# Optimization experiments

Measured on AMD Instinct MI355X. Metric: run time of the kernel, lower is better.

Reference implementation:

```python
import jax, jax.numpy as jnp
from jax import lax
import numpy as np

G, K = 8, 9  # deformable groups, 3x3 kernel taps


def conv1x1_bn_relu(x, W, scale, bias):
    # Conv2d 1x1 (no bias) + folded eval-mode BatchNorm (per-channel scale/bias) + ReLU
    y = jnp.einsum('bchw,oc->bohw', x, W)
    return jax.nn.relu(y * scale[None, :, None, None] + bias[None, :, None, None])


def dcn_v2(feat, offset_feat, W_om, b_om, W_dcn, b_dcn):
    # Modulated deformable conv v2, 3x3, stride 1, pad 1, dilation 1,
    # deformable_groups=G, extra_offset_mask: offsets/mask predicted from offset_feat.
    B, C, H, W_ = feat.shape
    Cg = C // G
    om = lax.conv_general_dilated(offset_feat, W_om, (1, 1), ((1, 1), (1, 1)))
    om = om + b_om[None, :, None, None]              # [B, 3*G*K, H, W]
    o1, o2, m = jnp.split(om, 3, axis=1)
    off_y = o1.reshape(B, G, K, H, W_)
    off_x = o2.reshape(B, G, K, H, W_)
    mask = jax.nn.sigmoid(m).reshape(B, G, K, H, W_)
    dk = jnp.arange(3) - 1
    dkh = jnp.repeat(dk, 3)   # tap row offset,  k = kh*3 + kw
    dkw = jnp.tile(dk, 3)     # tap col offset
    hh = jnp.arange(H, dtype=feat.dtype)
    ww = jnp.arange(W_, dtype=feat.dtype)
    py = hh[None, None, None, :, None] + dkh[None, None, :, None, None].astype(feat.dtype) + off_y
    px = ww[None, None, None, None, :] + dkw[None, None, :, None, None].astype(feat.dtype) + off_x
    y0 = jnp.floor(py); x0 = jnp.floor(px)
    ty = py - y0; tx = px - x0
    xg = feat.reshape(B, G, Cg, H * W_)

    def gather(idx):  # idx [B,G,K,H,W] int32 -> [B,G,Cg,K,H,W]
        f = lambda xf, i: xf[:, i]
        return jax.vmap(jax.vmap(f))(xg, idx)

    val = jnp.zeros((B, G, Cg, K, H, W_), dtype=feat.dtype)
    y0i = y0.astype(jnp.int32); x0i = x0.astype(jnp.int32)
    for dy, wy in ((0, 1.0 - ty), (1, ty)):
        iy = y0i + dy
        vy = (iy >= 0) & (iy < H)
        iyc = jnp.clip(iy, 0, H - 1)
        for dx, wx in ((0, 1.0 - tx), (1, tx)):
            ix = x0i + dx
            v = vy & (ix >= 0) & (ix < W_)
            idx = iyc * W_ + jnp.clip(ix, 0, W_ - 1)
            w = (wy * wx) * v.astype(feat.dtype)      # zero-padding outside
            val = val + w[:, :, None] * gather(idx)
    val = val * mask[:, :, None]                      # modulation
    Wd = W_dcn.reshape(W_dcn.shape[0], G, Cg, K)      # [Cout, G, Cg, K]
    out = jnp.einsum('bgckhw,ogck->bohw', val, Wd) + b_dcn[None, :, None, None]
    return out


def setup_inputs() -> dict:
    key = jax.random.key(0)
    ks = jax.random.split(key, 16)
    B, C, H, W_ = 8, 128, 64, 64
    Cd = C // 2  # dcn out channels = 64
    d = {}
    d['feat_l'] = jax.random.normal(ks[0], (B, C, H, W_), jnp.float32)
    d['feat_s'] = jax.random.normal(ks[1], (B, C, H // 2, W_ // 2), jnp.float32)
    d['W_fsm'] = jax.random.normal(ks[2], (C, C), jnp.float32) / np.sqrt(C)
    d['s_fsm'] = 1.0 + 0.1 * jax.random.normal(ks[3], (C,), jnp.float32)
    d['b_fsm'] = 0.1 * jax.random.normal(ks[4], (C,), jnp.float32)
    d['W_off'] = jax.random.normal(ks[5], (C, 2 * C), jnp.float32) / np.sqrt(2 * C)
    d['s_off'] = 1.0 + 0.1 * jax.random.normal(ks[6], (C,), jnp.float32)
    d['b_off'] = 0.1 * jax.random.normal(ks[7], (C,), jnp.float32)
    d['W_om'] = 0.05 * jax.random.normal(ks[8], (3 * G * K, C, 3, 3), jnp.float32)
    d['b_om'] = jnp.zeros((3 * G * K,), jnp.float32)
    d['W_dcn'] = jax.random.normal(ks[9], (Cd, C, 3, 3), jnp.float32) / np.sqrt(C * 9)
    d['b_dcn'] = 0.1 * jax.random.normal(ks[10], (Cd,), jnp.float32)
    d['W_cat'] = jax.random.normal(ks[11], (C, Cd), jnp.float32) / np.sqrt(Cd)
    d['s_cat'] = 1.0 + 0.1 * jax.random.normal(ks[12], (C,), jnp.float32)
    d['b_cat'] = 0.1 * jax.random.normal(ks[13], (C,), jnp.float32)
    return d


def reference(feat_l, feat_s, W_fsm, s_fsm, b_fsm, W_off, s_off, b_off,
              W_om, b_om, W_dcn, b_dcn, W_cat, s_cat, b_cat):
    # nearest upsample x2 (F.interpolate nearest to feat_l spatial size)
    feat_up = jnp.repeat(jnp.repeat(feat_s, 2, axis=2), 2, axis=3)
    feat_arm = conv1x1_bn_relu(feat_l, W_fsm, s_fsm, b_fsm)
    offset = conv1x1_bn_relu(jnp.concatenate([feat_arm, feat_up * 2.0], axis=1),
                             W_off, s_off, b_off)
    feat_align = jax.nn.relu(dcn_v2(feat_up, offset, W_om, b_om, W_dcn, b_dcn))
    feat = conv1x1_bn_relu(feat_align, W_cat, s_cat, b_cat) + feat_arm
    return (feat, feat_arm)
```

## Files before the change

### kernel.cpp

```cpp
#include <hip/hip_runtime.h>


typedef __attribute__((ext_vector_type(8))) short short8;
typedef __attribute__((ext_vector_type(4))) float f32x4;
typedef _Float16 __attribute__((ext_vector_type(2))) h2;

static __device__ __forceinline__ unsigned short f2bf(float x) {
    union { float f; unsigned int u; } v; v.f = x;
    return (unsigned short)((v.u + 0x7FFF + ((v.u >> 16) & 1)) >> 16);
}
static __device__ __forceinline__ unsigned short f2h(float x) {
    union { _Float16 h; unsigned short u; } v; v.h = (_Float16)x;
    return v.u;
}

__global__ __launch_bounds__(256) void k_prepfs(const float* __restrict__ fs,
        uint4* __restrict__ fsT4, uint4* __restrict__ fsH4) {
    __shared__ unsigned short st[64 * 136];
    unsigned int* st32 = (unsigned int*)st;
    const int t = threadIdx.x;
    const int b = blockIdx.x >> 4;
    const int p0 = (blockIdx.x & 15) << 6;
    for (int i = t; i < 64 * 64; i += 256) {
        int c2 = i >> 6, px = i & 63;
        float v0 = fs[(((b << 7) + 2 * c2) << 10) + p0 + px];
        float v1 = fs[(((b << 7) + 2 * c2 + 1) << 10) + p0 + px];
        st32[px * 68 + c2] = (unsigned int)f2bf(v0) | ((unsigned int)f2bf(v1) << 16);
    }
    __syncthreads();
    for (int i = t; i < 64 * 16; i += 256) {
        int px = i >> 4, q = i & 15;
        fsT4[(((b << 10) + p0 + px) << 4) + q] = ((const uint4*)(st + px * 136))[q];
    }
    __syncthreads();
    for (int i = t; i < 64 * 64; i += 256) {
        int c2 = i >> 6, px = i & 63;
        float v0 = fs[(((b << 7) + 2 * c2) << 10) + p0 + px];
        float v1 = fs[(((b << 7) + 2 * c2 + 1) << 10) + p0 + px];
        st32[px * 68 + c2] = (unsigned int)f2h(v0) | ((unsigned int)f2h(v1) << 16);
    }
    __syncthreads();
    for (int i = t; i < 64 * 16; i += 256) {
        int px = i >> 4, q = i & 15;
        fsH4[(((b << 10) + p0 + px) << 4) + q] = ((const uint4*)(st + px * 136))[q];
    }
}

__global__ __launch_bounds__(256) void k_packall(
        const float* __restrict__ W_fsm, const float* __restrict__ W_off,
        const float* __restrict__ W_cat, const float* __restrict__ W_dcn,
        const float* __restrict__ W_om,
        unsigned short* __restrict__ wbfsm, unsigned short* __restrict__ wboff,
        unsigned short* __restrict__ wbcat, unsigned short* __restrict__ wbdcn,
        unsigned short* __restrict__ wb2) {
    int idx = blockIdx.x * 256 + threadIdx.x;
    int lane = idx & 63;
    int ml = lane & 15, kl = (lane >> 4) * 8;
    unsigned short tmp[8];
    if (idx < 2048) {
        int r = idx >> 6;
        int o = (r % 8) * 16 + ml, k0 = (r / 8) * 32 + kl;
#pragma unroll
        for (int j = 0; j < 8; j++) tmp[j] = f2bf(W_fsm[o * 128 + k0 + j]);
        ((uint4*)wbfsm)[idx] = *(const uint4*)tmp;
    } else if (idx < 6144) {
        int i2 = idx - 2048;
        int r = i2 >> 6;
        int o = (r % 8) * 16 + ml, k0 = (r / 8) * 32 + kl;
#pragma unroll
        for (int j = 0; j < 8; j++) {
            int k = k0 + j;
            float f = W_off[o * 256 + k];
            if (k >= 128) f *= 2.0f;
            tmp[j] = f2bf(f);
        }
        ((uint4*)wboff)[i2] = *(const uint4*)tmp;
    } else if (idx < 7168) {
        int i2 = idx - 6144;
        int r = i2 >> 6;
        int o = (r % 8) * 16 + ml, k0 = (r / 8) * 32 + kl;
#pragma unroll
        for (int j = 0; j < 8; j++) tmp[j] = f2bf(W_cat[o * 64 + k0 + j]);
        ((uint4*)wbcat)[i2] = *(const uint4*)tmp;
    } else if (idx < 16384) {
        int i2 = idx - 7168;
        int r = i2 >> 6;
        int o = (r & 3) * 16 + ml, k0 = (r >> 2) * 32 + kl;
#pragma unroll
        for (int j = 0; j < 8; j++) {
            int k = k0 + j;
            int g = k / 144;
            int rem = k - g * 144;
            tmp[j] = f2h(W_dcn[(o * 128 + g * 16 + (rem & 15)) * 9 + (rem >> 4)]);
        }
        ((uint4*)wbdcn)[i2] = *(const uint4*)tmp;
    } else if (idx < 53248) {
        int i2 = idx - 16384;
        int r = i2 >> 6;
        int nt = r & 15, kk = r >> 4;
        int tap = kk >> 2, cc = kk & 3;
        int o = nt * 16 + ml;
        int c0 = cc * 32 + kl;
#pragma unroll
        for (int j = 0; j < 8; j++) {
            float v = (o < 216) ? W_om[(o * 128 + (c0 + j)) * 9 + tap] : 0.0f;
            tmp[j] = f2bf(v);
        }
        ((uint4*)wb2)[i2] = *(const uint4*)tmp;
    }
}

__global__ __launch_bounds__(256) void k12(const float* __restrict__ feat_l,
        const uint4* __restrict__ fsT4,
        const unsigned short* __restrict__ wbf, const unsigned short* __restrict__ wbo,
        const float* __restrict__ s_fsm, const float* __restrict__ b_fsm,
        const float* __restrict__ s_off, const float* __restrict__ b_off,
        float* __restrict__ feat_arm, unsigned short* __restrict__ offT) {
    __shared__ unsigned short A1[64 * 136];
    __shared__ unsigned short A2[64 * 264];
    float* E32 = (float*)A1;
    const int t = threadIdx.x;
    const int b = blockIdx.x >> 6;
    const int h = blockIdx.x & 63;
    const int hw0 = h << 6;
    unsigned int* A1w = (unsigned int*)A1;
    for (int i = t; i < 64 * 64; i += 256) {
        int c2 = i >> 6, px = i & 63;
        float v0 = feat_l[(((b << 7) + 2 * c2) << 12) + hw0 + px];
        float v1 = feat_l[(((b << 7) + 2 * c2 + 1) << 12) + hw0 + px];
        A1w[px * 68 + c2] = (unsigned int)f2bf(v0) | ((unsigned int)f2bf(v1) << 16);
    }
    {
        const int h2 = h >> 1;
        for (int i = t; i < 32 * 16; i += 256) {
            int px2 = i >> 4, q = i & 15;
            uint4 v = fsT4[(((b << 10) + (h2 << 5) + px2) << 4) + q];
            ((uint4*)(A2 + (2 * px2) * 264 + 128))[q] = v;
            ((uint4*)(A2 + (2 * px2 + 1) * 264 + 128))[q] = v;
        }
    }
    __syncthreads();
    const int lane = t & 63;
    const int wid = __builtin_amdgcn_readfirstlane(t >> 6);
    const int m = lane & 15, ko = lane >> 4;
    f32x4 acc[8];
#pragma unroll
    for (int nt = 0; nt < 8; nt++) acc[nt] = (f32x4){0.f, 0.f, 0.f, 0.f};
#pragma unroll
    for (int kk = 0; kk < 4; kk++) {
        short8 av = *(const short8*)(A1 + (wid * 16 + m) * 136 + kk * 32 + ko * 8);
        const uint4* wb = (const uint4*)wbf + (kk * 8) * 64 + lane;
#pragma unroll
        for (int nt = 0; nt < 8; nt++) {
            uint4 bu = wb[nt * 64];
            acc[nt] = __builtin_amdgcn_mfma_f32_16x16x32_bf16(av, *(short8*)&bu, acc[nt], 0, 0, 0);
        }
    }
#pragma unroll
    for (int nt = 0; nt < 8; nt++) {
        int o = nt * 16 + m;
        float sc = s_fsm[o], bi = b_fsm[o];
#pragma unroll
        for (int r = 0; r < 4; r++) {
            float v = fmaf(acc[nt][r], sc, bi);
            v = v > 0.f ? v : 0.f;
            acc[nt][r] = v;
            A2[(wid * 16 + ko * 4 + r) * 264 + o] = f2bf(v);
        }
    }
#pragma unroll 1
    for (int half = 0; half < 2; half++) {
        __syncthreads();
#pragma unroll
        for (int nt2 = 0; nt2 < 4; nt2++) {
            int nt = half * 4 + nt2;
#pragma unroll
            for (int r = 0; r < 4; r++)
                E32[(wid * 16 + ko * 4 + r) * 67 + nt2 * 16 + m] = acc[nt][r];
        }
        __syncthreads();
        for (int i = t; i < 4096; i += 256) {
            int ol = i >> 6, pp = i & 63;
            feat_arm[(((b << 7) + half * 64 + ol) << 12) + hw0 + pp] = E32[pp * 67 + ol];
        }
    }
    __syncthreads();
    f32x4 acc2[8];
#pragma unroll
    for (int nt = 0; nt < 8; nt++) acc2[nt] = (f32x4){0.f, 0.f, 0.f, 0.f};
#pragma unroll
    for (int kk = 0; kk < 8; kk++) {
        short8 av = *(const short8*)(A2 + (wid * 16 + m) * 264 + kk * 32 + ko * 8);
        const uint4* wb = (const uint4*)wbo + (kk * 8) * 64 + lane;
#pragma unroll
        for (int nt = 0; nt < 8; nt++) {
            uint4 bu = wb[nt * 64];
            acc2[nt] = __builtin_amdgcn_mfma_f32_16x16x32_bf16(av, *(short8*)&bu, acc2[nt], 0, 0, 0);
        }
    }
    __syncthreads();
#pragma unroll
    for (int nt = 0; nt < 8; nt++) {
        int o = nt * 16 + m;
        float sc = s_off[o], bi = b_off[o];
#pragma unroll
        for (int r = 0; r < 4; r++) {
            float v = fmaf(acc2[nt][r], sc, bi);
            v = v > 0.f ? v : 0.f;
            A2[(wid * 16 + ko * 4 + r) * 264 + o] = f2bf(v);
        }
    }
    __syncthreads();
    for (int i = t; i < 64 * 16; i += 256) {
        int px = i >> 4, q = i & 15;
        ((uint4*)offT)[(((b << 12) + hw0 + px) << 4) + q] = ((const uint4*)(A2 + px * 264))[q];
    }
}

__global__ __launch_bounds__(256, 2) void k_omdcn(
        const unsigned short* __restrict__ offT, const uint4* __restrict__ fsH4,
        const unsigned short* __restrict__ Wb2, const float* __restrict__ bom,
        const unsigned short* __restrict__ wbd, const float* __restrict__ bd,
        const unsigned short* __restrict__ wbc,
        const float* __restrict__ s_cat, const float* __restrict__ b_cat,
        const float* __restrict__ feat_arm, float* __restrict__ feat) {
    __shared__ float LDSf[16384];
    unsigned short* st = (unsigned short*)LDSf;
    float* omT = LDSf;
    unsigned short* A3 = (unsigned short*)(LDSf + 13888);
    float* T = LDSf;
    const uint4* offT4 = (const uint4*)offT;
    const uint4* W4 = (const uint4*)Wb2;
    const int t = threadIdx.x;
    const int b = blockIdx.x >> 6;
    const int h = blockIdx.x & 63;
    for (int i = t; i < 3 * 66 * 16; i += 256) {
        int q = i & 15;
        int rp = i >> 4;
        int r = rp / 66, p = rp - r * 66;
        int gy = h + r - 1, gx = p - 1;
        uint4 v = make_uint4(0, 0, 0, 0);
        if (gy >= 0 && gy < 64 && gx >= 0 && gx < 64)
            v = offT4[((((b << 6) + gy) << 6) + gx) * 16 + q];
        ((uint4*)(st + rp * 136))[q] = v;
    }
    __syncthreads();
    const int lane = t & 63;
    const int wid = __builtin_amdgcn_readfirstlane(t >> 6);
    const int m = lane & 15, ko = lane >> 4;
    f32x4 acc[16];
#pragma unroll
    for (int i = 0; i < 16; i++) acc[i] = (f32x4){0.f, 0.f, 0.f, 0.f};
#pragma unroll 4
    for (int kk = 0; kk < 36; kk++) {
        const int tap = kk >> 2, cc = kk & 3;
        const int dy = tap / 3, dx = tap - dy * 3;
        uint4 b4[4];
#pragma unroll
        for (int nt2 = 0; nt2 < 4; nt2++)
            b4[nt2] = W4[(((kk << 4) + (wid << 2) + nt2) << 6) + lane];
        short8 a8[4];
#pragma unroll
        for (int mt = 0; mt < 4; mt++) {
            int p = mt * 16 + m + dx;
            a8[mt] = *(const short8*)(st + (dy * 66 + p) * 136 + (cc << 5) + (ko << 3));
        }
#pragma unroll
        for (int nt2 = 0; nt2 < 4; nt2++)
#pragma unroll
            for (int mt = 0; mt < 4; mt++)
                acc[nt2 * 4 + mt] = __builtin_amdgcn_mfma_f32_16x16x32_bf16(
                    a8[mt], *(short8*)&b4[nt2], acc[nt2 * 4 + mt], 0, 0, 0);
    }
    __syncthreads();
#pragma unroll
    for (int nt2 = 0; nt2 < 4; nt2++) {
        int o = ((wid * 4 + nt2) << 4) + m;
        if (o < 216) {
            float bv = bom[o];
#pragma unroll
            for (int mt = 0; mt < 4; mt++) {
                f32x4 v = acc[nt2 * 4 + mt];
#pragma unroll
                for (int r = 0; r < 4; r++)
                    omT[(mt * 16 + (ko << 2) + r) * 217 + o] = v[r] + bv;
            }
        }
    }
    __syncthreads();
    const int px = (wid << 4) + m;
    const float fh = (float)h, fw = (float)px;
    const int pb_ = b << 10;
    const float* omrow = omT + px * 217;
    f32x4 accd[4];
#pragma unroll
    for (int nt = 0; nt < 4; nt++) accd[nt] = (f32x4){0.f, 0.f, 0.f, 0.f};
#pragma unroll
    for (int kk = 0; kk < 36; kk++) {
        int k0 = (kk << 5) + (ko << 3);
        int g = k0 / 144;
        int rem = k0 - g * 144;
        int tap = rem >> 4;
        int c0 = rem & 15;
        int ch = g * 9 + tap;
        float oy = omrow[ch];
        float ox = omrow[72 + ch];
        float mmv = omrow[144 + ch];
        mmv = 1.0f / (1.0f + __expf(-mmv));
        float py = fh + (float)(tap / 3 - 1) + oy;
        float pxx = fw + (float)(tap % 3 - 1) + ox;
        float y0f = floorf(py), x0f = floorf(pxx);
        float tyf = py - y0f, txf = pxx - x0f;
        int y0i = (int)y0f, x0i = (int)x0f;
        int y1i = y0i + 1, x1i = x0i + 1;
        bool vy0 = (y0i >= 0) && (y0i < 64);
        bool vy1 = (y1i >= 0) && (y1i < 64);
        bool vx0 = (x0i >= 0) && (x0i < 64);
        bool vx1 = (x1i >= 0) && (x1i < 64);
        float w00 = (vy0 && vx0) ? (1.0f - tyf) * (1.0f - txf) * mmv : 0.0f;
        float w01 = (vy0 && vx1) ? (1.0f - tyf) * txf * mmv : 0.0f;
        float w10 = (vy1 && vx0) ? tyf * (1.0f - txf) * mmv : 0.0f;
        float w11 = (vy1 && vx1) ? tyf * txf * mmv : 0.0f;
        int yc0 = y0i < 0 ? 0 : (y0i > 63 ? 63 : y0i);
        int yc1 = y1i < 0 ? 0 : (y1i > 63 ? 63 : y1i);
        int xc0 = x0i < 0 ? 0 : (x0i > 63 ? 63 : x0i);
        int xc1 = x1i < 0 ? 0 : (x1i > 63 ? 63 : x1i);
        int row0 = (yc0 >> 1) << 5, row1 = (yc1 >> 1) << 5;
        int ci = g * 2 + (c0 >> 3);
        union { uint4 u; h2 h[4]; } C00, C01, C10, C11;
        C00.u = fsH4[((pb_ + row0 + (xc0 >> 1)) << 4) + ci];
        C01.u = fsH4[((pb_ + row0 + (xc1 >> 1)) << 4) + ci];
        C10.u = fsH4[((pb_ + row1 + (xc0 >> 1)) << 4) + ci];
        C11.u = fsH4[((pb_ + row1 + (xc1 >> 1)) << 4) + ci];
        _Float16 h00 = (_Float16)w00, h01 = (_Float16)w01;
        _Float16 h10 = (_Float16)w10, h11 = (_Float16)w11;
        h2 W00 = (h2){h00, h00}, W01 = (h2){h01, h01};
        h2 W10 = (h2){h10, h10}, W11 = (h2){h11, h11};
        union { short8 s; h2 h[4]; } av;
#pragma unroll
        for (int c = 0; c < 4; c++)
            av.h[c] = C00.h[c] * W00 + C01.h[c] * W01 + C10.h[c] * W10 + C11.h[c] * W11;
        const uint4* wb = (const uint4*)wbd + (kk << 2) * 64 + lane;
#pragma unroll
        for (int nt = 0; nt < 4; nt++) {
            uint4 bu = wb[nt * 64];
            accd[nt] = __builtin_amdgcn_mfma_f32_16x16x32_f16(av.s, *(short8*)&bu, accd[nt], 0, 0, 0);
        }
    }
#pragma unroll
    for (int nt = 0; nt < 4; nt++) {
        int o = (nt << 4) + m;
        float bv = bd[o];
#pragma unroll
        for (int r = 0; r < 4; r++) {
            float v = accd[nt][r] + bv;
            v = v > 0.f ? v : 0.f;
            A3[((wid << 4) + (ko << 2) + r) * 72 + o] = f2bf(v);
        }
    }
    f32x4 acc2[8];
#pragma unroll
    for (int nt = 0; nt < 8; nt++) acc2[nt] = (f32x4){0.f, 0.f, 0.f, 0.f};
#pragma unroll
    for (int kk2 = 0; kk2 < 2; kk2++) {
        short8 av = *(const short8*)(A3 + ((wid << 4) + m) * 72 + kk2 * 32 + (ko << 3));
#pragma unroll
        for (int nt2 = 0; nt2 < 8; nt2++) {
            uint4 bu = ((const uint4*)wbc)[(kk2 * 8 + nt2) * 64 + lane];
            acc2[nt2] = __builtin_amdgcn_mfma_f32_16x16x32_bf16(av, *(short8*)&bu, acc2[nt2], 0, 0, 0);
        }
    }
#pragma unroll 1
    for (int half = 0; half < 2; half++) {
        __syncthreads();
#pragma unroll
        for (int nt2l = 0; nt2l < 4; nt2l++) {
            int nt2 = half * 4 + nt2l;
            int o = (nt2 << 4) + m;
            float sc = s_cat[o], bi = b_cat[o];
#pragma unroll
            for (int r = 0; r < 4; r++) {
                float v = fmaf(acc2[nt2][r], sc, bi);
                v = v > 0.f ? v : 0.f;
                T[((wid << 4) + (ko << 2) + r) * 67 + (nt2l << 4) + m] = v;
            }
        }
        __syncthreads();
        for (int i = t; i < 4096; i += 256) {
            int ol = i >> 6, pp = i & 63;
            int gidx = (((b << 7) + half * 64 + ol) << 12) + (h << 6) + pp;
            feat[gidx] = T[pp * 67 + ol] + feat_arm[gidx];
        }
    }
}

extern "C" void kernel_launch(void* const* d_in, const int* in_sizes, int n_in,
                              void* d_out, int out_size, void* d_ws, size_t ws_size,
                              hipStream_t stream) {
    const float* feat_l = (const float*)d_in[0];
    const float* feat_s = (const float*)d_in[1];
    const float* W_fsm  = (const float*)d_in[2];
    const float* s_fsm  = (const float*)d_in[3];
    const float* b_fsm  = (const float*)d_in[4];
    const float* W_off  = (const float*)d_in[5];
    const float* s_off  = (const float*)d_in[6];
    const float* b_off  = (const float*)d_in[7];
    const float* W_om   = (const float*)d_in[8];
    const float* b_om   = (const float*)d_in[9];
    const float* W_dcn  = (const float*)d_in[10];
    const float* b_dcn  = (const float*)d_in[11];
    const float* W_cat  = (const float*)d_in[12];
    const float* s_cat  = (const float*)d_in[13];
    const float* b_cat  = (const float*)d_in[14];

    float* feat     = (float*)d_out;
    float* feat_arm = feat + 4194304;

    float* ws = (float*)d_ws;
    unsigned short* offT = (unsigned short*)ws;
    uint4* fsT4  = (uint4*)(ws + 9175040);
    unsigned short* wb2   = (unsigned short*)(ws + 9699328);
    unsigned short* wbfsm = (unsigned short*)(ws + 9846784);
    unsigned short* wboff = (unsigned short*)(ws + 9854976);
    unsigned short* wbcat = (unsigned short*)(ws + 9871360);
    unsigned short* wbdcn = (unsigned short*)(ws + 9875456);
    uint4* fsH4  = (uint4*)(ws + 9912320);

    k_prepfs<<<128, 256, 0, stream>>>(feat_s, fsT4, fsH4);
    k_packall<<<208, 256, 0, stream>>>(W_fsm, W_off, W_cat, W_dcn, W_om,
                                       wbfsm, wboff, wbcat, wbdcn, wb2);

    k12<<<512, 256, 0, stream>>>(feat_l, fsT4, wbfsm, wboff,
                                 s_fsm, b_fsm, s_off, b_off, feat_arm, offT);
    k_omdcn<<<512, 256, 0, stream>>>(offT, fsH4, wb2, b_om, wbdcn, b_dcn,
                                     wbcat, s_cat, b_cat, feat_arm, feat);
}
```

Measured before the change: 188.0 us.

## Double block size to 512 threads with split-K and split-N wave partitioning

Both main kernels move from 256 to 512 threads per block. In k12 the extra waves split the output channels between two wave groups. In k_omdcn they split the K dimension of the offset conv and the deformable conv into halves, reduce partial sums through LDS, and split the N dimension of the final 1x1 conv. The aim is more waves per block to hide the latency of the gather and the MFMAs, and a shorter serial K loop per wave. In exchange it adds extra LDS reduction passes and barriers, and register limits under the launch bounds of (512,4) may cause spills.

Measured after the change: 176.2 us. -6.3%, faster.

```diff
diff --git a/kernel.cpp b/kernel.cpp
--- a/kernel.cpp
+++ b/kernel.cpp
@@ -110,7 +110,7 @@
     }
 }
 
-__global__ __launch_bounds__(256) void k12(const float* __restrict__ feat_l,
+__global__ __launch_bounds__(512, 4) void k12(const float* __restrict__ feat_l,
         const uint4* __restrict__ fsT4,
         const unsigned short* __restrict__ wbf, const unsigned short* __restrict__ wbo,
         const float* __restrict__ s_fsm, const float* __restrict__ b_fsm,
@@ -124,7 +124,7 @@
     const int h = blockIdx.x & 63;
     const int hw0 = h << 6;
     unsigned int* A1w = (unsigned int*)A1;
-    for (int i = t; i < 64 * 64; i += 256) {
+    for (int i = t; i < 64 * 64; i += 512) {
         int c2 = i >> 6, px = i & 63;
         float v0 = feat_l[(((b << 7) + 2 * c2) << 12) + hw0 + px];
         float v1 = feat_l[(((b << 7) + 2 * c2 + 1) << 12) + hw0 + px];
@@ -132,92 +132,92 @@
     }
     {
         const int h2 = h >> 1;
-        for (int i = t; i < 32 * 16; i += 256) {
-            int px2 = i >> 4, q = i & 15;
-            uint4 v = fsT4[(((b << 10) + (h2 << 5) + px2) << 4) + q];
-            ((uint4*)(A2 + (2 * px2) * 264 + 128))[q] = v;
-            ((uint4*)(A2 + (2 * px2 + 1) * 264 + 128))[q] = v;
-        }
+        int px2 = t >> 4, q = t & 15;
+        uint4 v = fsT4[(((b << 10) + (h2 << 5) + px2) << 4) + q];
+        ((uint4*)(A2 + (2 * px2) * 264 + 128))[q] = v;
+        ((uint4*)(A2 + (2 * px2 + 1) * 264 + 128))[q] = v;
     }
     __syncthreads();
     const int lane = t & 63;
-    const int wid = __builtin_amdgcn_readfirstlane(t >> 6);
+    const int w = __builtin_amdgcn_readfirstlane(t >> 6);
+    const int pq = w & 3;
+    const int nh = w >> 2;
     const int m = lane & 15, ko = lane >> 4;
-    f32x4 acc[8];
-#pragma unroll
-    for (int nt = 0; nt < 8; nt++) acc[nt] = (f32x4){0.f, 0.f, 0.f, 0.f};
+    f32x4 acc[4];
+#pragma unroll
+    for (int nt2 = 0; nt2 < 4; nt2++) acc[nt2] = (f32x4){0.f, 0.f, 0.f, 0.f};
 #pragma unroll
     for (int kk = 0; kk < 4; kk++) {
-        short8 av = *(const short8*)(A1 + (wid * 16 + m) * 136 + kk * 32 + ko * 8);
-        const uint4* wb = (const uint4*)wbf + (kk * 8) * 64 + lane;
-#pragma unroll
-        for (int nt = 0; nt < 8; nt++) {
-            uint4 bu = wb[nt * 64];
-            acc[nt] = __builtin_amdgcn_mfma_f32_16x16x32_bf16(av, *(short8*)&bu, acc[nt], 0, 0, 0);
-        }
-    }
-#pragma unroll
-    for (int nt = 0; nt < 8; nt++) {
-        int o = nt * 16 + m;
+        short8 av = *(const short8*)(A1 + (pq * 16 + m) * 136 + kk * 32 + ko * 8);
+        const uint4* wb = (const uint4*)wbf + (kk * 8 + nh * 4) * 64 + lane;
+#pragma unroll
+        for (int nt2 = 0; nt2 < 4; nt2++) {
+            uint4 bu = wb[nt2 * 64];
+            acc[nt2] = __builtin_amdgcn_mfma_f32_16x16x32_bf16(av, *(short8*)&bu, acc[nt2], 0, 0, 0);
+        }
+    }
+#pragma unroll
+    for (int nt2 = 0; nt2 < 4; nt2++) {
+        int o = ((nh << 2) + nt2) * 16 + m;
         float sc = s_fsm[o], bi = b_fsm[o];
 #pragma unroll
         for (int r = 0; r < 4; r++) {
-            float v = fmaf(acc[nt][r], sc, bi);
+            float v = fmaf(acc[nt2][r], sc, bi);
             v = v > 0.f ? v : 0.f;
-            acc[nt][r] = v;
-            A2[(wid * 16 + ko * 4 + r) * 264 + o] = f2bf(v);
+            acc[nt2][r] = v;
+            A2[(pq * 16 + ko * 4 + r) * 264 + o] = f2bf(v);
         }
     }
 #pragma unroll 1
     for (int half = 0; half < 2; half++) {
         __syncthreads();
-#pragma unroll
-        for (int nt2 = 0; nt2 < 4; nt2++) {
-            int nt = half * 4 + nt2;
-#pragma unroll
-            for (int r = 0; r < 4; r++)
-                E32[(wid * 16 + ko * 4 + r) * 67 + nt2 * 16 + m] = acc[nt][r];
+        if (nh == half) {
+#pragma unroll
+            for (int nt2 = 0; nt2 < 4; nt2++)
+#pragma unroll
+                for (int r = 0; r < 4; r++)
+                    E32[(pq * 16 + ko * 4 + r) * 67 + nt2 * 16 + m] = acc[nt2][r];
         }
         __syncthreads();
-        for (int i = t; i < 4096; i += 256) {
+        for (int i = t; i < 4096; i += 512) {
             int ol = i >> 6, pp = i & 63;
             feat_arm[(((b << 7) + half * 64 + ol) << 12) + hw0 + pp] = E32[pp * 67 + ol];
         }
     }
     __syncthreads();
-    f32x4 acc2[8];
-#pragma unroll
-    for (int nt = 0; nt < 8; nt++) acc2[nt] = (f32x4){0.f, 0.f, 0.f, 0.f};
+    f32x4 acc2[4];
+#pragma unroll
+    for (int nt2 = 0; nt2 < 4; nt2++) acc2[nt2] = (f32x4){0.f, 0.f, 0.f, 0.f};
 #pragma unroll
     for (int kk = 0; kk < 8; kk++) {
-        short8 av = *(const short8*)(A2 + (wid * 16 + m) * 264 + kk * 32 + ko * 8);
-        const uint4* wb = (const uint4*)wbo + (kk * 8) * 64 + lane;
-#pragma unroll
-        for (int nt = 0; nt < 8; nt++) {
-            uint4 bu = wb[nt * 64];
-            acc2[nt] = __builtin_amdgcn_mfma_f32_16x16x32_bf16(av, *(short8*)&bu, acc2[nt], 0, 0, 0);
-        }
-    }
-    __syncthreads();
-#pragma unroll
-    for (int nt = 0; nt < 8; nt++) {
-        int o = nt * 16 + m;
+        short8 av = *(const short8*)(A2 + (pq * 16 + m) * 264 + kk * 32 + ko * 8);
+        const uint4* wb = (const uint4*)wbo + (kk * 8 + nh * 4) * 64 + lane;
+#pragma unroll
+        for (int nt2 = 0; nt2 < 4; nt2++) {
+            uint4 bu = wb[nt2 * 64];
+            acc2[nt2] = __builtin_amdgcn_mfma_f32_16x16x32_bf16(av, *(short8*)&bu, acc2[nt2], 0, 0, 0);
+        }
+    }
+    __syncthreads();
+#pragma unroll
+    for (int nt2 = 0; nt2 < 4; nt2++) {
+        int o = ((nh << 2) + nt2) * 16 + m;
         float sc = s_off[o], bi = b_off[o];
 #pragma unroll
         for (int r = 0; r < 4; r++) {
-            float v = fmaf(acc2[nt][r], sc, bi);
+            float v = fmaf(acc2[nt2][r], sc, bi);
             v = v > 0.f ? v : 0.f;
-            A2[(wid * 16 + ko * 4 + r) * 264 + o] = f2bf(v);
-        }
-    }
-    __syncthreads();
-    for (int i = t; i < 64 * 16; i += 256) {
+            A2[(pq * 16 + ko * 4 + r) * 264 + o] = f2bf(v);
+        }
+    }
+    __syncthreads();
+    for (int i = t; i < 64 * 16; i += 512) {
         int px = i >> 4, q = i & 15;
         ((uint4*)offT)[(((b << 12) + hw0 + px) << 4) + q] = ((const uint4*)(A2 + px * 264))[q];
     }
 }
 
-__global__ __launch_bounds__(256, 2) void k_omdcn(
+__global__ __launch_bounds__(512, 4) void k_omdcn(
         const unsigned short* __restrict__ offT, const uint4* __restrict__ fsH4,
         const unsigned short* __restrict__ Wb2, const float* __restrict__ bom,
         const unsigned short* __restrict__ wbd, const float* __restrict__ bd,
@@ -227,6 +227,7 @@
     __shared__ float LDSf[16384];
     unsigned short* st = (unsigned short*)LDSf;
     float* omT = LDSf;
+    float* Rbuf = LDSf;
     unsigned short* A3 = (unsigned short*)(LDSf + 13888);
     float* T = LDSf;
     const uint4* offT4 = (const uint4*)offT;
@@ -234,7 +235,7 @@
     const int t = threadIdx.x;
     const int b = blockIdx.x >> 6;
     const int h = blockIdx.x & 63;
-    for (int i = t; i < 3 * 66 * 16; i += 256) {
+    for (int i = t; i < 3 * 66 * 16; i += 512) {
         int q = i & 15;
         int rp = i >> 4;
         int r = rp / 66, p = rp - r * 66;
@@ -246,147 +247,189 @@
     }
     __syncthreads();
     const int lane = t & 63;
-    const int wid = __builtin_amdgcn_readfirstlane(t >> 6);
+    const int w = __builtin_amdgcn_readfirstlane(t >> 6);
+    const int nq = w & 3;
+    const int kh = w >> 2;
     const int m = lane & 15, ko = lane >> 4;
     f32x4 acc[16];
 #pragma unroll
     for (int i = 0; i < 16; i++) acc[i] = (f32x4){0.f, 0.f, 0.f, 0.f};
+    {
+        const int kk0 = kh * 18;
 #pragma unroll 4
-    for (int kk = 0; kk < 36; kk++) {
-        const int tap = kk >> 2, cc = kk & 3;
-        const int dy = tap / 3, dx = tap - dy * 3;
-        uint4 b4[4];
-#pragma unroll
-        for (int nt2 = 0; nt2 < 4; nt2++)
-            b4[nt2] = W4[(((kk << 4) + (wid << 2) + nt2) << 6) + lane];
-        short8 a8[4];
-#pragma unroll
-        for (int mt = 0; mt < 4; mt++) {
-            int p = mt * 16 + m + dx;
-            a8[mt] = *(const short8*)(st + (dy * 66 + p) * 136 + (cc << 5) + (ko << 3));
-        }
-#pragma unroll
-        for (int nt2 = 0; nt2 < 4; nt2++)
-#pragma unroll
-            for (int mt = 0; mt < 4; mt++)
-                acc[nt2 * 4 + mt] = __builtin_amdgcn_mfma_f32_16x16x32_bf16(
-                    a8[mt], *(short8*)&b4[nt2], acc[nt2 * 4 + mt], 0, 0, 0);
-    }
-    __syncthreads();
-#pragma unroll
-    for (int nt2 = 0; nt2 < 4; nt2++) {
-        int o = ((wid * 4 + nt2) << 4) + m;
-        if (o < 216) {
-            float bv = bom[o];
+        for (int kki = 0; kki < 18; kki++) {
+            const int kk = kk0 + kki;
+            const int tap = kk >> 2, cc = kk & 3;
+            const int dy = tap / 3, dx = tap - dy * 3;
+            uint4 b4[4];
+#pragma unroll
+            for (int nt2 = 0; nt2 < 4; nt2++)
+                b4[nt2] = W4[(((kk << 4) + (nq << 2) + nt2) << 6) + lane];
+            short8 a8[4];
 #pragma unroll
             for (int mt = 0; mt < 4; mt++) {
-                f32x4 v = acc[nt2 * 4 + mt];
-#pragma unroll
-                for (int r = 0; r < 4; r++)
-                    omT[(mt * 16 + (ko << 2) + r) * 217 + o] = v[r] + bv;
-            }
-        }
-    }
-    __syncthreads();
-    const int px = (wid << 4) + m;
+                int p = mt * 16 + m + dx;
+                a8[mt] = *(const short8*)(st + (dy * 66 + p) * 136 + (cc << 5) + (ko << 3));
+            }
+#pragma unroll
+            for (int nt2 = 0; nt2 < 4; nt2++)
+#pragma unroll
+                for (int mt = 0; mt < 4; mt++)
+                    acc[nt2 * 4 + mt] = __builtin_amdgcn_mfma_f32_16x16x32_bf16(
+                        a8[mt], *(short8*)&b4[nt2], acc[nt2 * 4 + mt], 0, 0, 0);
+        }
+    }
+    __syncthreads();
+    if (kh == 0) {
+#pragma unroll
+        for (int nt2 = 0; nt2 < 4; nt2++) {
+            int o = ((nq << 2) + nt2) * 16 + m;
+            if (o < 216) {
+                float bv = bom[o];
+#pragma unroll
+                for (int mt = 0; mt < 4; mt++) {
+                    f32x4 v = acc[nt2 * 4 + mt];
+#pragma unroll
+                    for (int r = 0; r < 4; r++)
+                        omT[(mt * 16 + (ko << 2) + r) * 217 + o] = v[r] + bv;
+                }
+            }
+        }
+    }
+    __syncthreads();
+    if (kh == 1) {
+#pragma unroll
+        for (int nt2 = 0; nt2 < 4; nt2++) {
+            int o = ((nq << 2) + nt2) * 16 + m;
+            if (o < 216) {
+#pragma unroll
+                for (int mt = 0; mt < 4; mt++) {
+                    f32x4 v = acc[nt2 * 4 + mt];
+#pragma unroll
+                    for (int r = 0; r < 4; r++)
+                        omT[(mt * 16 + (ko << 2) + r) * 217 + o] += v[r];
+                }
+            }
+        }
+    }
+    __syncthreads();
+    const int px = (nq << 4) + m;
     const float fh = (float)h, fw = (float)px;
     const int pb_ = b << 10;
     const float* omrow = omT + px * 217;
     f32x4 accd[4];
 #pragma unroll
     for (int nt = 0; nt < 4; nt++) accd[nt] = (f32x4){0.f, 0.f, 0.f, 0.f};
-#pragma unroll
-    for (int kk = 0; kk < 36; kk++) {
-        int k0 = (kk << 5) + (ko << 3);
-        int g = k0 / 144;
-        int rem = k0 - g * 144;
-        int tap = rem >> 4;
-        int c0 = rem & 15;
-        int ch = g * 9 + tap;
-        float oy = omrow[ch];
-        float ox = omrow[72 + ch];
-        float mmv = omrow[144 + ch];
-        mmv = 1.0f / (1.0f + __expf(-mmv));
-        float py = fh + (float)(tap / 3 - 1) + oy;
-        float pxx = fw + (float)(tap % 3 - 1) + ox;
-        float y0f = floorf(py), x0f = floorf(pxx);
-        float tyf = py - y0f, txf = pxx - x0f;
-        int y0i = (int)y0f, x0i = (int)x0f;
-        int y1i = y0i + 1, x1i = x0i + 1;
-        bool vy0 = (y0i >= 0) && (y0i < 64);
-        bool vy1 = (y1i >= 0) && (y1i < 64);
-        bool vx0 = (x0i >= 0) && (x0i < 64);
-        bool vx1 = (x1i >= 0) && (x1i < 64);
-        float w00 = (vy0 && vx0) ? (1.0f - tyf) * (1.0f - txf) * mmv : 0.0f;
-        float w01 = (vy0 && vx1) ? (1.0f - tyf) * txf * mmv : 0.0f;
-        float w10 = (vy1 && vx0) ? tyf * (1.0f - txf) * mmv : 0.0f;
-        float w11 = (vy1 && vx1) ? tyf * txf * mmv : 0.0f;
-        int yc0 = y0i < 0 ? 0 : (y0i > 63 ? 63 : y0i);
-        int yc1 = y1i < 0 ? 0 : (y1i > 63 ? 63 : y1i);
-        int xc0 = x0i < 0 ? 0 : (x0i > 63 ? 63 : x0i);
-        int xc1 = x1i < 0 ? 0 : (x1i > 63 ? 63 : x1i);
-        int row0 = (yc0 >> 1) << 5, row1 = (yc1 >> 1) << 5;
-        int ci = g * 2 + (c0 >> 3);
-        union { uint4 u; h2 h[4]; } C00, C01, C10, C11;
-        C00.u = fsH4[((pb_ + row0 + (xc0 >> 1)) << 4) + ci];
-        C01.u = fsH4[((pb_ + row0 + (xc1 >> 1)) << 4) + ci];
-        C10.u = fsH4[((pb_ + row1 + (xc0 >> 1)) << 4) + ci];
-        C11.u = fsH4[((pb_ + row1 + (xc1 >> 1)) << 4) + ci];
-        _Float16 h00 = (_Float16)w00, h01 = (_Float16)w01;
-        _Float16 h10 = (_Float16)w10, h11 = (_Float16)w11;
-        h2 W00 = (h2){h00, h00}, W01 = (h2){h01, h01};
-        h2 W10 = (h2){h10, h10}, W11 = (h2){h11, h11};
-        union { short8 s; h2 h[4]; } av;
-#pragma unroll
-        for (int c = 0; c < 4; c++)
-            av.h[c] = C00.h[c] * W00 + C01.h[c] * W01 + C10.h[c] * W10 + C11.h[c] * W11;
-        const uint4* wb = (const uint4*)wbd + (kk << 2) * 64 + lane;
+    {
+        const int dk0 = kh * 18;
+#pragma unroll
+        for (int kki = 0; kki < 18; kki++) {
+            const int kk = dk0 + kki;
+            int k0 = (kk << 5) + (ko << 3);
+            int g = k0 / 144;
+            int rem = k0 - g * 144;
+            int tap = rem >> 4;
+            int c0 = rem & 15;
+            int ch = g * 9 + tap;
+            float oy = omrow[ch];
+            float ox = omrow[72 + ch];
+            float mmv = omrow[144 + ch];
+            mmv = 1.0f / (1.0f + __expf(-mmv));
+            float py = fh + (float)(tap / 3 - 1) + oy;
+            float pxx = fw + (float)(tap % 3 - 1) + ox;
+            float y0f = floorf(py), x0f = floorf(pxx);
+            float tyf = py - y0f, txf = pxx - x0f;
+            int y0i = (int)y0f, x0i = (int)x0f;
+            int y1i = y0i + 1, x1i = x0i + 1;
+            bool vy0 = (y0i >= 0) && (y0i < 64);
+            bool vy1 = (y1i >= 0) && (y1i < 64);
+            bool vx0 = (x0i >= 0) && (x0i < 64);
+            bool vx1 = (x1i >= 0) && (x1i < 64);
+            float w00 = (vy0 && vx0) ? (1.0f - tyf) * (1.0f - txf) * mmv : 0.0f;
+            float w01 = (vy0 && vx1) ? (1.0f - tyf) * txf * mmv : 0.0f;
+            float w10 = (vy1 && vx0) ? tyf * (1.0f - txf) * mmv : 0.0f;
+            float w11 = (vy1 && vx1) ? tyf * txf * mmv : 0.0f;
+            int yc0 = y0i < 0 ? 0 : (y0i > 63 ? 63 : y0i);
+            int yc1 = y1i < 0 ? 0 : (y1i > 63 ? 63 : y1i);
+            int xc0 = x0i < 0 ? 0 : (x0i > 63 ? 63 : x0i);
+            int xc1 = x1i < 0 ? 0 : (x1i > 63 ? 63 : x1i);
+            int row0 = (yc0 >> 1) << 5, row1 = (yc1 >> 1) << 5;
+            int ci = g * 2 + (c0 >> 3);
+            union { uint4 u; h2 h[4]; } C00, C01, C10, C11;
+            C00.u = fsH4[((pb_ + row0 + (xc0 >> 1)) << 4) + ci];
+            C01.u = fsH4[((pb_ + row0 + (xc1 >> 1)) << 4) + ci];
+            C10.u = fsH4[((pb_ + row1 + (xc0 >> 1)) << 4) + ci];
+            C11.u = fsH4[((pb_ + row1 + (xc1 >> 1)) << 4) + ci];
+            _Float16 h00 = (_Float16)w00, h01 = (_Float16)w01;
+            _Float16 h10 = (_Float16)w10, h11 = (_Float16)w11;
+            h2 W00 = (h2){h00, h00}, W01 = (h2){h01, h01};
+            h2 W10 = (h2){h10, h10}, W11 = (h2){h11, h11};
+            union { short8 s; h2 h[4]; } av;
+#pragma unroll
+            for (int c = 0; c < 4; c++)
+                av.h[c] = C00.h[c] * W00 + C01.h[c] * W01 + C10.h[c] * W10 + C11.h[c] * W11;
+            const uint4* wb = (const uint4*)wbd + (kk << 2) * 64 + lane;
+#pragma unroll
+            for (int nt = 0; nt < 4; nt++) {
+                uint4 bu = wb[nt * 64];
+                accd[nt] = __builtin_amdgcn_mfma_f32_16x16x32_f16(av.s, *(short8*)&bu, accd[nt], 0, 0, 0);
+            }
+        }
+    }
+    __syncthreads();
+    if (kh == 1) {
+#pragma unroll
+        for (int nt = 0; nt < 4; nt++)
+            *(f32x4*)(Rbuf + ((nq << 6) + lane) * 20 + (nt << 2)) = accd[nt];
+    }
+    __syncthreads();
+    if (kh == 0) {
+#pragma unroll
+        for (int nt = 0; nt < 4; nt++)
+            accd[nt] += *(const f32x4*)(Rbuf + ((nq << 6) + lane) * 20 + (nt << 2));
 #pragma unroll
         for (int nt = 0; nt < 4; nt++) {
-            uint4 bu = wb[nt * 64];
-            accd[nt] = __builtin_amdgcn_mfma_f32_16x16x32_f16(av.s, *(short8*)&bu, accd[nt], 0, 0, 0);
-        }
-    }
-#pragma unroll
-    for (int nt = 0; nt < 4; nt++) {
-        int o = (nt << 4) + m;
-        float bv = bd[o];
-#pragma unroll
-        for (int r = 0; r < 4; r++) {
-            float v = accd[nt][r] + bv;
-            v = v > 0.f ? v : 0.f;
-            A3[((wid << 4) + (ko << 2) + r) * 72 + o] = f2bf(v);
-        }
-    }
-    f32x4 acc2[8];
-#pragma unroll
-    for (int nt = 0; nt < 8; nt++) acc2[nt] = (f32x4){0.f, 0.f, 0.f, 0.f};
+            int o = (nt << 4) + m;
+            float bv = bd[o];
+#pragma unroll
+            for (int r = 0; r < 4; r++) {
+                float v = accd[nt][r] + bv;
+                v = v > 0.f ? v : 0.f;
+                A3[((nq << 4) + (ko << 2) + r) * 72 + o] = f2bf(v);
+            }
+        }
+    }
+    __syncthreads();
+    f32x4 acc2[4];
+#pragma unroll
+    for (int nt2 = 0; nt2 < 4; nt2++) acc2[nt2] = (f32x4){0.f, 0.f, 0.f, 0.f};
 #pragma unroll
     for (int kk2 = 0; kk2 < 2; kk2++) {
-        short8 av = *(const short8*)(A3 + ((wid << 4) + m) * 72 + kk2 * 32 + (ko << 3));
-#pragma unroll
-        for (int nt2 = 0; nt2 < 8; nt2++) {
-            uint4 bu = ((const uint4*)wbc)[(kk2 * 8 + nt2) * 64 + lane];
+        short8 av = *(const short8*)(A3 + ((nq << 4) + m) * 72 + kk2 * 32 + (ko << 3));
+#pragma unroll
+        for (int nt2 = 0; nt2 < 4; nt2++) {
+            uint4 bu = ((const uint4*)wbc)[(kk2 * 8 + (kh << 2) + nt2) * 64 + lane];
             acc2[nt2] = __builtin_amdgcn_mfma_f32_16x16x32_bf16(av, *(short8*)&bu, acc2[nt2], 0, 0, 0);
         }
     }
 #pragma unroll 1
     for (int half = 0; half < 2; half++) {
         __syncthreads();
-#pragma unroll
-        for (int nt2l = 0; nt2l < 4; nt2l++) {
-            int nt2 = half * 4 + nt2l;
-            int o = (nt2 << 4) + m;
-            float sc = s_cat[o], bi = b_cat[o];
-#pragma unroll
-            for (int r = 0; r < 4; r++) {
-                float v = fmaf(acc2[nt2][r], sc, bi);
-                v = v > 0.f ? v : 0.f;
-                T[((wid << 4) + (ko << 2) + r) * 67 + (nt2l << 4) + m] = v;
+        if (kh == half) {
+#pragma unroll
+            for (int nt2 = 0; nt2 < 4; nt2++) {
+                int o = (((kh << 2) + nt2) << 4) + m;
+                float sc = s_cat[o], bi = b_cat[o];
+#pragma unroll
+                for (int r = 0; r < 4; r++) {
+                    float v = fmaf(acc2[nt2][r], sc, bi);
+                    v = v > 0.f ? v : 0.f;
+                    T[((nq << 4) + (ko << 2) + r) * 67 + (nt2 << 4) + m] = v;
+                }
             }
         }
         __syncthreads();
-        for (int i = t; i < 4096; i += 256) {
+        for (int i = t; i < 4096; i += 512) {
             int ol = i >> 6, pp = i & 63;
             int gidx = (((b << 7) + half * 64 + ol) << 12) + (h << 6) + pp;
             feat[gidx] = T[pp * 67 + ol] + feat_arm[gidx];
@@ -430,8 +473,8 @@
     k_packall<<<208, 256, 0, stream>>>(W_fsm, W_off, W_cat, W_dcn, W_om,
                                        wbfsm, wboff, wbcat, wbdcn, wb2);
 
-    k12<<<512, 256, 0, stream>>>(feat_l, fsT4, wbfsm, wboff,
+    k12<<<512, 512, 0, stream>>>(feat_l, fsT4, wbfsm, wboff,
                                  s_fsm, b_fsm, s_off, b_off, feat_arm, offT);
-    k_omdcn<<<512, 256, 0, stream>>>(offT, fsH4, wb2, b_om, wbdcn, b_dcn,
+    k_omdcn<<<512, 512, 0, stream>>>(offT, fsH4, wb2, b_om, wbdcn, b_dcn,
                                      wbcat, s_cat, b_cat, feat_arm, feat);
 }
```
